# Kernel tuning notes

Hardware: AMD Instinct MI355X
Metric: run time of the kernel (lower is better)

## Reference

```python
import jax, jax.numpy as jnp
import numpy as np

OUT_H = 7
OUT_W = 7
SPATIAL_SCALE = 0.0625
SAMPLING_RATIO = 2  # grid points per bin edge (static, as in Detectron2 configs)
ALIGNED = True


def setup_inputs() -> dict:
    key = jax.random.key(0)
    k_feat, k_xy, k_b = jax.random.split(key, 3)
    N, C, H, W = 2, 256, 128, 128
    K = 1024
    feat = jax.random.normal(k_feat, (N, C, H, W), dtype=jnp.float32)
    img = H / SPATIAL_SCALE  # 2048.0, image-space extent
    # two random corners per axis, sorted -> valid boxes in image coords
    xy = jax.random.uniform(k_xy, (K, 2, 2), dtype=jnp.float32) * img  # [K, {x,y}, 2]
    lo = jnp.min(xy, axis=-1)
    hi = jnp.max(xy, axis=-1)
    b = jax.random.randint(k_b, (K,), 0, N).astype(jnp.float32)
    rois = jnp.stack([b, lo[:, 0], lo[:, 1], hi[:, 0], hi[:, 1]], axis=1)  # [K,5]
    return {"feat": feat, "rois": rois}


def _roi_align(feat, rois):
    N, C, H, W = feat.shape
    K = rois.shape[0]
    g = SAMPLING_RATIO
    b = rois[:, 0].astype(jnp.int32)
    off = 0.5 if ALIGNED else 0.0
    x1 = rois[:, 1] * SPATIAL_SCALE - off
    y1 = rois[:, 2] * SPATIAL_SCALE - off
    x2 = rois[:, 3] * SPATIAL_SCALE - off
    y2 = rois[:, 4] * SPATIAL_SCALE - off
    rw = x2 - x1
    rh = y2 - y1
    if not ALIGNED:  # legacy: force min size 1
        rw = jnp.maximum(rw, 1.0)
        rh = jnp.maximum(rh, 1.0)
    bin_w = rw / OUT_W
    bin_h = rh / OUT_H
    # sample offsets within a bin: (i + 0.5)/g for i in 0..g-1
    frac = (jnp.arange(g, dtype=feat.dtype) + 0.5) / g  # [g]
    ph = jnp.arange(OUT_H, dtype=feat.dtype)
    pw = jnp.arange(OUT_W, dtype=feat.dtype)
    ys = y1[:, None, None] + (ph[None, :, None] + frac[None, None, :]) * bin_h[:, None, None]  # [K,PH,g]
    xs = x1[:, None, None] + (pw[None, :, None] + frac[None, None, :]) * bin_w[:, None, None]  # [K,PW,g]
    ys = ys.reshape(K, OUT_H * g)  # [K,Sy]
    xs = xs.reshape(K, OUT_W * g)  # [K,Sx]
    Y = jnp.broadcast_to(ys[:, :, None], (K, OUT_H * g, OUT_W * g))
    X = jnp.broadcast_to(xs[:, None, :], (K, OUT_H * g, OUT_W * g))
    S = OUT_H * g * OUT_W * g
    Y = Y.reshape(K, S)
    X = X.reshape(K, S)
    valid = (Y > -1.0) & (Y < H) & (X > -1.0) & (X < W)
    Yc = jnp.maximum(Y, 0.0)
    Xc = jnp.maximum(X, 0.0)
    y0 = jnp.clip(jnp.floor(Yc).astype(jnp.int32), 0, H - 1)
    x0 = jnp.clip(jnp.floor(Xc).astype(jnp.int32), 0, W - 1)
    y1i = jnp.minimum(y0 + 1, H - 1)
    x1i = jnp.minimum(x0 + 1, W - 1)
    ly = jnp.clip(Yc - y0.astype(feat.dtype), 0.0, 1.0)
    lx = jnp.clip(Xc - x0.astype(feat.dtype), 0.0, 1.0)
    hy = 1.0 - ly
    hx = 1.0 - lx
    bI = b[:, None]  # [K,1] broadcasts against [K,S]
    # advanced indices around the channel slice put (K,S) in front -> [K,S,C]
    v00 = feat[bI, :, y0, x0]
    v01 = feat[bI, :, y0, x1i]
    v10 = feat[bI, :, y1i, x0]
    v11 = feat[bI, :, y1i, x1i]
    w00 = (hy * hx)[:, :, None]
    w01 = (hy * lx)[:, :, None]
    w10 = (ly * hx)[:, :, None]
    w11 = (ly * lx)[:, :, None]
    val = w00 * v00 + w01 * v01 + w10 * v10 + w11 * v11  # [K,S,C]
    val = jnp.where(valid[:, :, None], val, 0.0)
    val = val.reshape(K, OUT_H, g, OUT_W, g, C)
    out = val.mean(axis=(2, 4))  # avg pool over the g*g samples per bin
    return out.transpose(0, 3, 1, 2)  # [K,C,OUT_H,OUT_W]


def reference(feat, rois):
    return _roi_align(feat, rois)
```

## Files before the change

### kernel.cpp

```cpp
#include <hip/hip_runtime.h>
#include <hip/hip_fp16.h>

#define NIMG 2
#define CCH 256
#define FH 128
#define FW 128
#define FHW (FH * FW)
#define OUTH 7
#define OUTW 7
#define NPIX 49
#define NSAMP (NPIX * 4)
#define KROIS 1024
#define SCALE 0.0625f
#define OPITCH 260

typedef float f32x4 __attribute__((ext_vector_type(4)));

__global__ __launch_bounds__(1024) void sort_rois(const float* __restrict__ rois,
                                                  int* __restrict__ perm) {
    __shared__ int hist[128];
    __shared__ int basep[128];
    const int t = threadIdx.x;
    if (t < 128) hist[t] = 0;
    __syncthreads();
    const float* r = rois + t * 5;
    const int b = (int)r[0];
    const float cx = (r[1] + r[3]) * 0.5f * SCALE;
    const float cy = (r[2] + r[4]) * 0.5f * SCALE;
    const int qx = min(max((int)cx, 0), FW - 1) >> 4;
    const int qy = min(max((int)cy, 0), FH - 1) >> 4;
    unsigned m = 0;
#pragma unroll
    for (int i = 0; i < 3; ++i)
        m |= (((unsigned)(qx >> i) & 1u) << (2 * i)) | (((unsigned)(qy >> i) & 1u) << (2 * i + 1));
    const int key = (b << 6) | (int)m;
    const int rank = atomicAdd(&hist[key], 1);
    __syncthreads();
    if (t < 64) {
        const int a = hist[2 * t], c = hist[2 * t + 1];
        int s = a + c;
#pragma unroll
        for (int d = 1; d < 64; d <<= 1) {
            const int n = __shfl_up(s, d);
            if (t >= d) s += n;
        }
        const int excl = s - (a + c);
        basep[2 * t]     = excl;
        basep[2 * t + 1] = excl + a;
    }
    __syncthreads();
    perm[basep[key] + rank] = t;
}

__global__ __launch_bounds__(256) void nchw_to_nhwc_h(const float* __restrict__ in,
                                                      __half* __restrict__ out) {
    __shared__ float tile[32][33];
    const int b   = blockIdx.z;
    const int hw0 = blockIdx.x << 5;
    const int c0  = blockIdx.y << 5;
    const int tx  = threadIdx.x;
    const int ty  = threadIdx.y;
    const float* src = in  + (size_t)b * CCH * FHW;
    __half*      dst = out + (size_t)b * FHW * CCH;
#pragma unroll
    for (int i = 0; i < 32; i += 8)
        tile[ty + i][tx] = src[(size_t)(c0 + ty + i) * FHW + hw0 + tx];
    __syncthreads();
#pragma unroll
    for (int i = 0; i < 32; i += 8)
        dst[(size_t)(hw0 + ty + i) * CCH + c0 + tx] = __float2half(tile[tx][ty + i]);
}

__global__ __launch_bounds__(512) void roi_align_nhwc(const __half* __restrict__ nhwc,
                                                      const float* __restrict__ rois,
                                                      const int* __restrict__ perm,
                                                      float* __restrict__ out) {
    __shared__ __half obuf[NPIX * OPITCH];
    __shared__ __align__(16) int   soff[NSAMP][4];
    __shared__ __align__(16) float swgt[NSAMP][4];
    const int wg = blockIdx.x;
    const int k = perm[((wg & 7) << 7) | (wg >> 3)];
    const int lane = threadIdx.x & 63;
    const int wave = threadIdx.x >> 6;
    const int t = threadIdx.x;

    const float* r = rois + k * 5;
    const int b = __builtin_amdgcn_readfirstlane((int)r[0]);

    if (t < NSAMP) {
        const float x1 = __fsub_rn(__fmul_rn(r[1], SCALE), 0.5f);
        const float y1 = __fsub_rn(__fmul_rn(r[2], SCALE), 0.5f);
        const float x2 = __fsub_rn(__fmul_rn(r[3], SCALE), 0.5f);
        const float y2 = __fsub_rn(__fmul_rn(r[4], SCALE), 0.5f);
        const float bw = __fdiv_rn(__fsub_rn(x2, x1), (float)OUTW);
        const float bh = __fdiv_rn(__fsub_rn(y2, y1), (float)OUTH);
        const int pix = t >> 2, s = t & 3;
        const int ph = pix / 7, pw = pix - ph * 7;
        const int sy = s >> 1, sx = s & 1;
        const float fy = (float)ph + (sy ? 0.75f : 0.25f);
        const float fx = (float)pw + (sx ? 0.75f : 0.25f);
        const float y = __fadd_rn(y1, __fmul_rn(fy, bh));
        const float x = __fadd_rn(x1, __fmul_rn(fx, bw));
        int o00 = 0, o01 = 0, o10 = 0, o11 = 0;
        float w00 = 0.f, w01 = 0.f, w10 = 0.f, w11 = 0.f;
        if (y > -1.0f && y < (float)FH && x > -1.0f && x < (float)FW) {
            const float yc = fmaxf(y, 0.0f);
            const float xc = fmaxf(x, 0.0f);
            int y0 = (int)yc; if (y0 > FH - 1) y0 = FH - 1;
            int x0 = (int)xc; if (x0 > FW - 1) x0 = FW - 1;
            const int y1i = min(y0 + 1, FH - 1);
            const int x1i = min(x0 + 1, FW - 1);
            const float ly = fminf(yc - (float)y0, 1.0f);
            const float lx = fminf(xc - (float)x0, 1.0f);
            const float hy = 1.0f - ly, hx = 1.0f - lx;
            w00 = hy * hx; w01 = hy * lx; w10 = ly * hx; w11 = ly * lx;
            o00 = (y0  * FW + x0 ) << 9;
            o01 = (y0  * FW + x1i) << 9;
            o10 = (y1i * FW + x0 ) << 9;
            o11 = (y1i * FW + x1i) << 9;
        }
        soff[t][0] = o00; soff[t][1] = o01; soff[t][2] = o10; soff[t][3] = o11;
        swgt[t][0] = w00; swgt[t][1] = w01; swgt[t][2] = w10; swgt[t][3] = w11;
    }
    __syncthreads();

    const char* bp = (const char*)(nhwc + ((size_t)b * FHW << 8)) + (lane << 3);
    for (int pix = wave; pix < NPIX; pix += 8) {
        float acc0 = 0.f, acc1 = 0.f, acc2 = 0.f, acc3 = 0.f;
#pragma unroll
        for (int s = 0; s < 4; ++s) {
            const int j = (pix << 2) + s;
            const int4  o = *(const int4*)(&soff[j][0]);
            const f32x4 w = *(const f32x4*)(&swgt[j][0]);
            const uint2 r00 = *(const uint2*)(bp + o.x);
            const uint2 r01 = *(const uint2*)(bp + o.y);
            const uint2 r10 = *(const uint2*)(bp + o.z);
            const uint2 r11 = *(const uint2*)(bp + o.w);
            const __half2 A00 = *(const __half2*)&r00.x, B00 = *(const __half2*)&r00.y;
            const __half2 A01 = *(const __half2*)&r01.x, B01 = *(const __half2*)&r01.y;
            const __half2 A10 = *(const __half2*)&r10.x, B10 = *(const __half2*)&r10.y;
            const __half2 A11 = *(const __half2*)&r11.x, B11 = *(const __half2*)&r11.y;
            acc0 = fmaf(w.x, __half2float(A00.x), acc0);
            acc1 = fmaf(w.x, __half2float(A00.y), acc1);
            acc2 = fmaf(w.x, __half2float(B00.x), acc2);
            acc3 = fmaf(w.x, __half2float(B00.y), acc3);
            acc0 = fmaf(w.y, __half2float(A01.x), acc0);
            acc1 = fmaf(w.y, __half2float(A01.y), acc1);
            acc2 = fmaf(w.y, __half2float(B01.x), acc2);
            acc3 = fmaf(w.y, __half2float(B01.y), acc3);
            acc0 = fmaf(w.z, __half2float(A10.x), acc0);
            acc1 = fmaf(w.z, __half2float(A10.y), acc1);
            acc2 = fmaf(w.z, __half2float(B10.x), acc2);
            acc3 = fmaf(w.z, __half2float(B10.y), acc3);
            acc0 = fmaf(w.w, __half2float(A11.x), acc0);
            acc1 = fmaf(w.w, __half2float(A11.y), acc1);
            acc2 = fmaf(w.w, __half2float(B11.x), acc2);
            acc3 = fmaf(w.w, __half2float(B11.y), acc3);
        }
        const __half2 h01 = __floats2half2_rn(acc0 * 0.25f, acc1 * 0.25f);
        const __half2 h23 = __floats2half2_rn(acc2 * 0.25f, acc3 * 0.25f);
        uint2 packed;
        packed.x = *(const unsigned*)&h01;
        packed.y = *(const unsigned*)&h23;
        *(uint2*)&obuf[pix * OPITCH + (lane << 2)] = packed;
    }
    __syncthreads();

    float* op = out + (size_t)k * (CCH * NPIX);
    for (int f4 = threadIdx.x; f4 < (CCH * NPIX) / 4; f4 += 512) {
        const int f = f4 << 2;
        f32x4 o;
        {
            const int fi = f + 0; const int c = fi / NPIX; const int p = fi - c * NPIX;
            o.x = __half2float(obuf[p * OPITCH + c]);
        }
        {
            const int fi = f + 1; const int c = fi / NPIX; const int p = fi - c * NPIX;
            o.y = __half2float(obuf[p * OPITCH + c]);
        }
        {
            const int fi = f + 2; const int c = fi / NPIX; const int p = fi - c * NPIX;
            o.z = __half2float(obuf[p * OPITCH + c]);
        }
        {
            const int fi = f + 3; const int c = fi / NPIX; const int p = fi - c * NPIX;
            o.w = __half2float(obuf[p * OPITCH + c]);
        }
        __builtin_nontemporal_store(o, (f32x4*)(op + f));
    }
}

__global__ __launch_bounds__(256) void roi_align_naive(const float* __restrict__ feat,
                                                       const float* __restrict__ rois,
                                                       float* __restrict__ out) {
    const size_t idx = (size_t)blockIdx.x * 256 + threadIdx.x;
    const size_t total = (size_t)KROIS * CCH * NPIX;
    if (idx >= total) return;
    const int pix = (int)(idx % NPIX);
    const int t1  = (int)(idx / NPIX);
    const int c   = t1 % CCH;
    const int k   = t1 / CCH;
    const int ph = pix / 7;
    const int pw = pix - ph * 7;

    const float* r = rois + k * 5;
    const int b = (int)r[0];
    const float x1 = __fsub_rn(__fmul_rn(r[1], SCALE), 0.5f);
    const float y1 = __fsub_rn(__fmul_rn(r[2], SCALE), 0.5f);
    const float x2 = __fsub_rn(__fmul_rn(r[3], SCALE), 0.5f);
    const float y2 = __fsub_rn(__fmul_rn(r[4], SCALE), 0.5f);
    const float bw = __fdiv_rn(__fsub_rn(x2, x1), (float)OUTW);
    const float bh = __fdiv_rn(__fsub_rn(y2, y1), (float)OUTH);
    const float* fp = feat + (size_t)(b * CCH + c) * FHW;

    float acc = 0.f;
#pragma unroll
    for (int s = 0; s < 4; ++s) {
        const int sy = s >> 1, sx = s & 1;
        const float fy = (float)ph + (sy ? 0.75f : 0.25f);
        const float fx = (float)pw + (sx ? 0.75f : 0.25f);
        const float y = __fadd_rn(y1, __fmul_rn(fy, bh));
        const float x = __fadd_rn(x1, __fmul_rn(fx, bw));
        if (y > -1.0f && y < (float)FH && x > -1.0f && x < (float)FW) {
            const float yc = fmaxf(y, 0.0f);
            const float xc = fmaxf(x, 0.0f);
            int y0 = (int)yc; if (y0 > FH - 1) y0 = FH - 1;
            int x0 = (int)xc; if (x0 > FW - 1) x0 = FW - 1;
            const int y1i = min(y0 + 1, FH - 1);
            const int x1i = min(x0 + 1, FW - 1);
            const float ly = fminf(yc - (float)y0, 1.0f);
            const float lx = fminf(xc - (float)x0, 1.0f);
            const float hy = 1.0f - ly, hx = 1.0f - lx;
            acc += (hy * hx) * fp[y0  * FW + x0 ] + (hy * lx) * fp[y0  * FW + x1i]
                 + (ly * hx) * fp[y1i * FW + x0 ] + (ly * lx) * fp[y1i * FW + x1i];
        }
    }
    out[idx] = acc * 0.25f;
}

extern "C" void kernel_launch(void* const* d_in, const int* in_sizes, int n_in,
                              void* d_out, int out_size, void* d_ws, size_t ws_size,
                              hipStream_t stream) {
    const float* feat = (const float*)d_in[0];
    const float* rois = (const float*)d_in[1];
    float* out = (float*)d_out;

    const size_t nhwc_bytes = (size_t)NIMG * CCH * FHW * sizeof(__half);
    const size_t need = nhwc_bytes + KROIS * sizeof(int);
    if (ws_size >= need) {
        __half* nhwc = (__half*)d_ws;
        int* perm = (int*)((char*)d_ws + nhwc_bytes);
        sort_rois<<<dim3(1), dim3(KROIS), 0, stream>>>(rois, perm);
        dim3 tg(FHW / 32, CCH / 32, NIMG);
        nchw_to_nhwc_h<<<tg, dim3(32, 8), 0, stream>>>(feat, nhwc);
        roi_align_nhwc<<<dim3(KROIS), dim3(512), 0, stream>>>(nhwc, rois, perm, out);
    } else {
        const size_t total = (size_t)KROIS * CCH * NPIX;
        roi_align_naive<<<dim3((unsigned)((total + 255) / 256)), dim3(256), 0, stream>>>(feat, rois, out);
    }
}
```

Baseline: 48.75 us.

## Fuse ROI sort into transpose kernel and process two ROIs per block

Merges the single-block ROI sort and the NCHW→NHWC half transpose into one launch, with the sort running in an extra block of 256 threads that handle four ROIs each. The ROI-align kernel now processes two consecutive sorted ROIs per block (512 blocks), and its per-wave pixel assignment changes from strided to contiguous ranges of six or seven pixels. The goal is to cut one kernel launch and the per-block setup cost. In exchange, each block adds barriers and runs its two ROIs serially, and fewer blocks are launched.

```diff
diff --git a/kernel.cpp b/kernel.cpp
--- a/kernel.cpp
+++ b/kernel.cpp
@@ -16,59 +16,73 @@
 
 typedef float f32x4 __attribute__((ext_vector_type(4)));
 
-__global__ __launch_bounds__(1024) void sort_rois(const float* __restrict__ rois,
+__global__ __launch_bounds__(256) void prep_fused(const float* __restrict__ in,
+                                                  __half* __restrict__ out,
+                                                  const float* __restrict__ rois,
                                                   int* __restrict__ perm) {
-    __shared__ int hist[128];
-    __shared__ int basep[128];
+    const int bid = blockIdx.x;
     const int t = threadIdx.x;
-    if (t < 128) hist[t] = 0;
-    __syncthreads();
-    const float* r = rois + t * 5;
-    const int b = (int)r[0];
-    const float cx = (r[1] + r[3]) * 0.5f * SCALE;
-    const float cy = (r[2] + r[4]) * 0.5f * SCALE;
-    const int qx = min(max((int)cx, 0), FW - 1) >> 4;
-    const int qy = min(max((int)cy, 0), FH - 1) >> 4;
-    unsigned m = 0;
-#pragma unroll
-    for (int i = 0; i < 3; ++i)
-        m |= (((unsigned)(qx >> i) & 1u) << (2 * i)) | (((unsigned)(qy >> i) & 1u) << (2 * i + 1));
-    const int key = (b << 6) | (int)m;
-    const int rank = atomicAdd(&hist[key], 1);
-    __syncthreads();
-    if (t < 64) {
-        const int a = hist[2 * t], c = hist[2 * t + 1];
-        int s = a + c;
-#pragma unroll
-        for (int d = 1; d < 64; d <<= 1) {
-            const int n = __shfl_up(s, d);
-            if (t >= d) s += n;
-        }
-        const int excl = s - (a + c);
-        basep[2 * t]     = excl;
-        basep[2 * t + 1] = excl + a;
-    }
-    __syncthreads();
-    perm[basep[key] + rank] = t;
-}
-
-__global__ __launch_bounds__(256) void nchw_to_nhwc_h(const float* __restrict__ in,
-                                                      __half* __restrict__ out) {
-    __shared__ float tile[32][33];
-    const int b   = blockIdx.z;
-    const int hw0 = blockIdx.x << 5;
-    const int c0  = blockIdx.y << 5;
-    const int tx  = threadIdx.x;
-    const int ty  = threadIdx.y;
-    const float* src = in  + (size_t)b * CCH * FHW;
-    __half*      dst = out + (size_t)b * FHW * CCH;
-#pragma unroll
-    for (int i = 0; i < 32; i += 8)
-        tile[ty + i][tx] = src[(size_t)(c0 + ty + i) * FHW + hw0 + tx];
-    __syncthreads();
-#pragma unroll
-    for (int i = 0; i < 32; i += 8)
-        dst[(size_t)(hw0 + ty + i) * CCH + c0 + tx] = __float2half(tile[tx][ty + i]);
+    if (bid < 8192) {
+        __shared__ float tile[32][33];
+        const int b   = bid >> 12;
+        const int rem = bid & 4095;
+        const int c0  = (rem >> 9) << 5;
+        const int hw0 = (rem & 511) << 5;
+        const int tx = t & 31;
+        const int ty = t >> 5;
+        const float* src = in  + (size_t)b * CCH * FHW;
+        __half*      dst = out + (size_t)b * FHW * CCH;
+#pragma unroll
+        for (int i = 0; i < 32; i += 8)
+            tile[ty + i][tx] = src[(size_t)(c0 + ty + i) * FHW + hw0 + tx];
+        __syncthreads();
+#pragma unroll
+        for (int i = 0; i < 32; i += 8)
+            dst[(size_t)(hw0 + ty + i) * CCH + c0 + tx] = __float2half(tile[tx][ty + i]);
+    } else {
+        __shared__ int hist[128];
+        __shared__ int basep[128];
+        __shared__ int keyv[KROIS];
+        __shared__ int rankv[KROIS];
+        if (t < 128) hist[t] = 0;
+        __syncthreads();
+#pragma unroll
+        for (int i = 0; i < 4; ++i) {
+            const int roi = t + (i << 8);
+            const float* r = rois + roi * 5;
+            const int b = (int)r[0];
+            const float cx = (r[1] + r[3]) * 0.5f * SCALE;
+            const float cy = (r[2] + r[4]) * 0.5f * SCALE;
+            const int qx = min(max((int)cx, 0), FW - 1) >> 4;
+            const int qy = min(max((int)cy, 0), FH - 1) >> 4;
+            unsigned m = 0;
+#pragma unroll
+            for (int j = 0; j < 3; ++j)
+                m |= (((unsigned)(qx >> j) & 1u) << (2 * j)) | (((unsigned)(qy >> j) & 1u) << (2 * j + 1));
+            const int key = (b << 6) | (int)m;
+            keyv[roi] = key;
+            rankv[roi] = atomicAdd(&hist[key], 1);
+        }
+        __syncthreads();
+        if (t < 64) {
+            const int a = hist[2 * t], c = hist[2 * t + 1];
+            int s = a + c;
+#pragma unroll
+            for (int d = 1; d < 64; d <<= 1) {
+                const int n = __shfl_up(s, d);
+                if (t >= d) s += n;
+            }
+            const int excl = s - (a + c);
+            basep[2 * t]     = excl;
+            basep[2 * t + 1] = excl + a;
+        }
+        __syncthreads();
+#pragma unroll
+        for (int i = 0; i < 4; ++i) {
+            const int roi = t + (i << 8);
+            perm[basep[keyv[roi]] + rankv[roi]] = roi;
+        }
+    }
 }
 
 __global__ __launch_bounds__(512) void roi_align_nhwc(const __half* __restrict__ nhwc,
@@ -79,114 +93,120 @@
     __shared__ __align__(16) int   soff[NSAMP][4];
     __shared__ __align__(16) float swgt[NSAMP][4];
     const int wg = blockIdx.x;
-    const int k = perm[((wg & 7) << 7) | (wg >> 3)];
+    const int pairBase = ((((wg & 7) << 6) | (wg >> 3)) << 1);
     const int lane = threadIdx.x & 63;
     const int wave = threadIdx.x >> 6;
     const int t = threadIdx.x;
 
-    const float* r = rois + k * 5;
-    const int b = __builtin_amdgcn_readfirstlane((int)r[0]);
-
-    if (t < NSAMP) {
-        const float x1 = __fsub_rn(__fmul_rn(r[1], SCALE), 0.5f);
-        const float y1 = __fsub_rn(__fmul_rn(r[2], SCALE), 0.5f);
-        const float x2 = __fsub_rn(__fmul_rn(r[3], SCALE), 0.5f);
-        const float y2 = __fsub_rn(__fmul_rn(r[4], SCALE), 0.5f);
-        const float bw = __fdiv_rn(__fsub_rn(x2, x1), (float)OUTW);
-        const float bh = __fdiv_rn(__fsub_rn(y2, y1), (float)OUTH);
-        const int pix = t >> 2, s = t & 3;
-        const int ph = pix / 7, pw = pix - ph * 7;
-        const int sy = s >> 1, sx = s & 1;
-        const float fy = (float)ph + (sy ? 0.75f : 0.25f);
-        const float fx = (float)pw + (sx ? 0.75f : 0.25f);
-        const float y = __fadd_rn(y1, __fmul_rn(fy, bh));
-        const float x = __fadd_rn(x1, __fmul_rn(fx, bw));
-        int o00 = 0, o01 = 0, o10 = 0, o11 = 0;
-        float w00 = 0.f, w01 = 0.f, w10 = 0.f, w11 = 0.f;
-        if (y > -1.0f && y < (float)FH && x > -1.0f && x < (float)FW) {
-            const float yc = fmaxf(y, 0.0f);
-            const float xc = fmaxf(x, 0.0f);
-            int y0 = (int)yc; if (y0 > FH - 1) y0 = FH - 1;
-            int x0 = (int)xc; if (x0 > FW - 1) x0 = FW - 1;
-            const int y1i = min(y0 + 1, FH - 1);
-            const int x1i = min(x0 + 1, FW - 1);
-            const float ly = fminf(yc - (float)y0, 1.0f);
-            const float lx = fminf(xc - (float)x0, 1.0f);
-            const float hy = 1.0f - ly, hx = 1.0f - lx;
-            w00 = hy * hx; w01 = hy * lx; w10 = ly * hx; w11 = ly * lx;
-            o00 = (y0  * FW + x0 ) << 9;
-            o01 = (y0  * FW + x1i) << 9;
-            o10 = (y1i * FW + x0 ) << 9;
-            o11 = (y1i * FW + x1i) << 9;
-        }
-        soff[t][0] = o00; soff[t][1] = o01; soff[t][2] = o10; soff[t][3] = o11;
-        swgt[t][0] = w00; swgt[t][1] = w01; swgt[t][2] = w10; swgt[t][3] = w11;
-    }
-    __syncthreads();
-
-    const char* bp = (const char*)(nhwc + ((size_t)b * FHW << 8)) + (lane << 3);
-    for (int pix = wave; pix < NPIX; pix += 8) {
-        float acc0 = 0.f, acc1 = 0.f, acc2 = 0.f, acc3 = 0.f;
-#pragma unroll
-        for (int s = 0; s < 4; ++s) {
-            const int j = (pix << 2) + s;
-            const int4  o = *(const int4*)(&soff[j][0]);
-            const f32x4 w = *(const f32x4*)(&swgt[j][0]);
-            const uint2 r00 = *(const uint2*)(bp + o.x);
-            const uint2 r01 = *(const uint2*)(bp + o.y);
-            const uint2 r10 = *(const uint2*)(bp + o.z);
-            const uint2 r11 = *(const uint2*)(bp + o.w);
-            const __half2 A00 = *(const __half2*)&r00.x, B00 = *(const __half2*)&r00.y;
-            const __half2 A01 = *(const __half2*)&r01.x, B01 = *(const __half2*)&r01.y;
-            const __half2 A10 = *(const __half2*)&r10.x, B10 = *(const __half2*)&r10.y;
-            const __half2 A11 = *(const __half2*)&r11.x, B11 = *(const __half2*)&r11.y;
-            acc0 = fmaf(w.x, __half2float(A00.x), acc0);
-            acc1 = fmaf(w.x, __half2float(A00.y), acc1);
-            acc2 = fmaf(w.x, __half2float(B00.x), acc2);
-            acc3 = fmaf(w.x, __half2float(B00.y), acc3);
-            acc0 = fmaf(w.y, __half2float(A01.x), acc0);
-            acc1 = fmaf(w.y, __half2float(A01.y), acc1);
-            acc2 = fmaf(w.y, __half2float(B01.x), acc2);
-            acc3 = fmaf(w.y, __half2float(B01.y), acc3);
-            acc0 = fmaf(w.z, __half2float(A10.x), acc0);
-            acc1 = fmaf(w.z, __half2float(A10.y), acc1);
-            acc2 = fmaf(w.z, __half2float(B10.x), acc2);
-            acc3 = fmaf(w.z, __half2float(B10.y), acc3);
-            acc0 = fmaf(w.w, __half2float(A11.x), acc0);
-            acc1 = fmaf(w.w, __half2float(A11.y), acc1);
-            acc2 = fmaf(w.w, __half2float(B11.x), acc2);
-            acc3 = fmaf(w.w, __half2float(B11.y), acc3);
-        }
-        const __half2 h01 = __floats2half2_rn(acc0 * 0.25f, acc1 * 0.25f);
-        const __half2 h23 = __floats2half2_rn(acc2 * 0.25f, acc3 * 0.25f);
-        uint2 packed;
-        packed.x = *(const unsigned*)&h01;
-        packed.y = *(const unsigned*)&h23;
-        *(uint2*)&obuf[pix * OPITCH + (lane << 2)] = packed;
-    }
-    __syncthreads();
-
-    float* op = out + (size_t)k * (CCH * NPIX);
-    for (int f4 = threadIdx.x; f4 < (CCH * NPIX) / 4; f4 += 512) {
-        const int f = f4 << 2;
-        f32x4 o;
-        {
-            const int fi = f + 0; const int c = fi / NPIX; const int p = fi - c * NPIX;
-            o.x = __half2float(obuf[p * OPITCH + c]);
-        }
-        {
-            const int fi = f + 1; const int c = fi / NPIX; const int p = fi - c * NPIX;
-            o.y = __half2float(obuf[p * OPITCH + c]);
-        }
-        {
-            const int fi = f + 2; const int c = fi / NPIX; const int p = fi - c * NPIX;
-            o.z = __half2float(obuf[p * OPITCH + c]);
-        }
-        {
-            const int fi = f + 3; const int c = fi / NPIX; const int p = fi - c * NPIX;
-            o.w = __half2float(obuf[p * OPITCH + c]);
-        }
-        __builtin_nontemporal_store(o, (f32x4*)(op + f));
+    for (int half = 0; half < 2; ++half) {
+        const int k = perm[pairBase + half];
+        const float* r = rois + k * 5;
+        const int b = __builtin_amdgcn_readfirstlane((int)r[0]);
+
+        if (t < NSAMP) {
+            const float x1 = __fsub_rn(__fmul_rn(r[1], SCALE), 0.5f);
+            const float y1 = __fsub_rn(__fmul_rn(r[2], SCALE), 0.5f);
+            const float x2 = __fsub_rn(__fmul_rn(r[3], SCALE), 0.5f);
+            const float y2 = __fsub_rn(__fmul_rn(r[4], SCALE), 0.5f);
+            const float bw = __fdiv_rn(__fsub_rn(x2, x1), (float)OUTW);
+            const float bh = __fdiv_rn(__fsub_rn(y2, y1), (float)OUTH);
+            const int pix = t >> 2, s = t & 3;
+            const int ph = pix / 7, pw = pix - ph * 7;
+            const int sy = s >> 1, sx = s & 1;
+            const float fy = (float)ph + (sy ? 0.75f : 0.25f);
+            const float fx = (float)pw + (sx ? 0.75f : 0.25f);
+            const float y = __fadd_rn(y1, __fmul_rn(fy, bh));
+            const float x = __fadd_rn(x1, __fmul_rn(fx, bw));
+            int o00 = 0, o01 = 0, o10 = 0, o11 = 0;
+            float w00 = 0.f, w01 = 0.f, w10 = 0.f, w11 = 0.f;
+            if (y > -1.0f && y < (float)FH && x > -1.0f && x < (float)FW) {
+                const float yc = fmaxf(y, 0.0f);
+                const float xc = fmaxf(x, 0.0f);
+                int y0 = (int)yc; if (y0 > FH - 1) y0 = FH - 1;
+                int x0 = (int)xc; if (x0 > FW - 1) x0 = FW - 1;
+                const int y1i = min(y0 + 1, FH - 1);
+                const int x1i = min(x0 + 1, FW - 1);
+                const float ly = fminf(yc - (float)y0, 1.0f);
+                const float lx = fminf(xc - (float)x0, 1.0f);
+                const float hy = 1.0f - ly, hx = 1.0f - lx;
+                w00 = hy * hx; w01 = hy * lx; w10 = ly * hx; w11 = ly * lx;
+                o00 = (y0  * FW + x0 ) << 9;
+                o01 = (y0  * FW + x1i) << 9;
+                o10 = (y1i * FW + x0 ) << 9;
+                o11 = (y1i * FW + x1i) << 9;
+            }
+            soff[t][0] = o00; soff[t][1] = o01; soff[t][2] = o10; soff[t][3] = o11;
+            swgt[t][0] = w00; swgt[t][1] = w01; swgt[t][2] = w10; swgt[t][3] = w11;
+        }
+        __syncthreads();
+
+        const char* bp = (const char*)(nhwc + ((size_t)b * FHW << 8)) + (lane << 3);
+        const int pstart = wave ? (6 * wave + 1) : 0;
+        const int pend   = 6 * wave + 6;
+        for (int pix = pstart; pix <= pend; ++pix) {
+            float acc0 = 0.f, acc1 = 0.f, acc2 = 0.f, acc3 = 0.f;
+#pragma unroll
+            for (int s = 0; s < 4; ++s) {
+                const int j = (pix << 2) + s;
+                const int4  o = *(const int4*)(&soff[j][0]);
+                const f32x4 w = *(const f32x4*)(&swgt[j][0]);
+                const uint2 r00 = *(const uint2*)(bp + o.x);
+                const uint2 r01 = *(const uint2*)(bp + o.y);
+                const uint2 r10 = *(const uint2*)(bp + o.z);
+                const uint2 r11 = *(const uint2*)(bp + o.w);
+                const __half2 A00 = *(const __half2*)&r00.x, B00 = *(const __half2*)&r00.y;
+                const __half2 A01 = *(const __half2*)&r01.x, B01 = *(const __half2*)&r01.y;
+                const __half2 A10 = *(const __half2*)&r10.x, B10 = *(const __half2*)&r10.y;
+                const __half2 A11 = *(const __half2*)&r11.x, B11 = *(const __half2*)&r11.y;
+                acc0 = fmaf(w.x, __half2float(A00.x), acc0);
+                acc1 = fmaf(w.x, __half2float(A00.y), acc1);
+                acc2 = fmaf(w.x, __half2float(B00.x), acc2);
+                acc3 = fmaf(w.x, __half2float(B00.y), acc3);
+                acc0 = fmaf(w.y, __half2float(A01.x), acc0);
+                acc1 = fmaf(w.y, __half2float(A01.y), acc1);
+                acc2 = fmaf(w.y, __half2float(B01.x), acc2);
+                acc3 = fmaf(w.y, __half2float(B01.y), acc3);
+                acc0 = fmaf(w.z, __half2float(A10.x), acc0);
+                acc1 = fmaf(w.z, __half2float(A10.y), acc1);
+                acc2 = fmaf(w.z, __half2float(B10.x), acc2);
+                acc3 = fmaf(w.z, __half2float(B10.y), acc3);
+                acc0 = fmaf(w.w, __half2float(A11.x), acc0);
+                acc1 = fmaf(w.w, __half2float(A11.y), acc1);
+                acc2 = fmaf(w.w, __half2float(B11.x), acc2);
+                acc3 = fmaf(w.w, __half2float(B11.y), acc3);
+            }
+            const __half2 h01 = __floats2half2_rn(acc0 * 0.25f, acc1 * 0.25f);
+            const __half2 h23 = __floats2half2_rn(acc2 * 0.25f, acc3 * 0.25f);
+            uint2 packed;
+            packed.x = *(const unsigned*)&h01;
+            packed.y = *(const unsigned*)&h23;
+            *(uint2*)&obuf[pix * OPITCH + (lane << 2)] = packed;
+        }
+        __syncthreads();
+
+        float* op = out + (size_t)k * (CCH * NPIX);
+        for (int f4 = t; f4 < (CCH * NPIX) / 4; f4 += 512) {
+            const int f = f4 << 2;
+            f32x4 o;
+            {
+                const int fi = f + 0; const int c = fi / NPIX; const int p = fi - c * NPIX;
+                o.x = __half2float(obuf[p * OPITCH + c]);
+            }
+            {
+                const int fi = f + 1; const int c = fi / NPIX; const int p = fi - c * NPIX;
+                o.y = __half2float(obuf[p * OPITCH + c]);
+            }
+            {
+                const int fi = f + 2; const int c = fi / NPIX; const int p = fi - c * NPIX;
+                o.z = __half2float(obuf[p * OPITCH + c]);
+            }
+            {
+                const int fi = f + 3; const int c = fi / NPIX; const int p = fi - c * NPIX;
+                o.w = __half2float(obuf[p * OPITCH + c]);
+            }
+            __builtin_nontemporal_store(o, (f32x4*)(op + f));
+        }
+        __syncthreads();
     }
 }
 
@@ -250,10 +270,8 @@
     if (ws_size >= need) {
         __half* nhwc = (__half*)d_ws;
         int* perm = (int*)((char*)d_ws + nhwc_bytes);
-        sort_rois<<<dim3(1), dim3(KROIS), 0, stream>>>(rois, perm);
-        dim3 tg(FHW / 32, CCH / 32, NIMG);
-        nchw_to_nhwc_h<<<tg, dim3(32, 8), 0, stream>>>(feat, nhwc);
-        roi_align_nhwc<<<dim3(KROIS), dim3(512), 0, stream>>>(nhwc, rois, perm, out);
+        prep_fused<<<dim3(8193), dim3(256), 0, stream>>>(feat, nhwc, rois, perm);
+        roi_align_nhwc<<<dim3(512), dim3(512), 0, stream>>>(nhwc, rois, perm, out);
     } else {
         const size_t total = (size_t)KROIS * CCH * NPIX;
         roi_align_naive<<<dim3((unsigned)((total + 255) / 256)), dim3(256), 0, stream>>>(feat, rois, out);
```

After: 48.60 us. Within noise of the previous version (-0.3%).
